# Kernel tuning notes

Measured on AMD Instinct MI355X. Metric: run time of the kernel, lower is better.

## Reference

```python
import jax, jax.numpy as jnp
import numpy as np

MARGIN = 0.4
GAMMA = 80.0
N = 4096
C = 64


def setup_inputs() -> dict:
    key = jax.random.key(0)
    k1, k2 = jax.random.split(key)
    similarity_matrix = jnp.tanh(jax.random.normal(k1, (N, N), dtype=jnp.float32))
    cluster_ids = jax.random.randint(k2, (N,), 0, C)
    clusters = jax.nn.one_hot(cluster_ids, C, dtype=jnp.float32)  # [N, C]
    return {"similarity_matrix": similarity_matrix, "clusters": clusters}


def reference(similarity_matrix, clusters):
    n = similarity_matrix.shape[0]
    # pairwise label dot products; original loop uses .item() -> detached weights
    prob = jax.lax.stop_gradient(clusters @ clusters.T)  # [n, n]
    upper = jnp.triu(jnp.ones((n, n), dtype=bool), k=1)
    pos = upper & (prob > 0)
    neg = upper & (prob <= 0)

    sim = similarity_matrix
    sim_d = jax.lax.stop_gradient(sim)
    ap = jnp.maximum(-sim_d + 1.0 + MARGIN, 0.0)
    an = jnp.maximum(sim_d + MARGIN, 0.0)
    delta_p = 1.0 - MARGIN
    delta_n = MARGIN
    logit_p = -ap * (sim - delta_p) * GAMMA
    logit_n = an * (sim - delta_n) * GAMMA

    neg_inf = jnp.float32(-jnp.inf)
    lse_p = jax.scipy.special.logsumexp(jnp.where(pos, logit_p, neg_inf))
    lse_n = jax.scipy.special.logsumexp(jnp.where(neg, logit_n, neg_inf))

    cnt_p = jnp.maximum(jnp.sum(pos), 1)
    cnt_n = jnp.maximum(jnp.sum(neg), 1)
    wp_mean = jnp.sum(jnp.where(pos, prob, 0.0)) / cnt_p
    wn_mean = jnp.sum(jnp.where(neg, prob, 0.0)) / cnt_n

    # mean over pairs of wp*softplus(lse_p) + wn*softplus(lse_n)
    loss = wp_mean * jax.nn.softplus(lse_p) + wn_mean * jax.nn.softplus(lse_n)
    return loss
```

## Files before the change

kernel.cpp:

```cpp
#include <hip/hip_runtime.h>
#include <math.h>

#define NN 4096
#define CC 64
#define CAP 256
#define QS 8
#define K3_THREADS 128

constexpr float K_MARGIN = 0.4f;
constexpr float K_GAMMA  = 80.0f;
constexpr float M_P = 307.2f;


__global__ void zero_kernel(int* __restrict__ cnt) {
    if (threadIdx.x < CC) cnt[threadIdx.x] = 0;
}

__global__ __launch_bounds__(256) void ids_bucket_kernel(const float* __restrict__ clusters,
                                                         int* __restrict__ cnt,
                                                         unsigned short* __restrict__ members) {
    const int row  = (blockIdx.x * 256 + threadIdx.x) >> 6;
    const int lane = threadIdx.x & 63;
    const float v = clusters[row * CC + lane];
    const unsigned long long m = __ballot(v > 0.5f);
    if (lane == 0) {
        const int id   = (int)__builtin_ctzll(m);
        const int slot = atomicAdd(&cnt[id], 1);
        members[id * CAP + slot] = (unsigned short)row;
    }
}

__global__ __launch_bounds__(K3_THREADS) void pairs_kernel(const float* __restrict__ sim,
                                                           const int* __restrict__ cnt,
                                                           const unsigned short* __restrict__ members,
                                                           float* __restrict__ partials) {
    const int c = blockIdx.x >> 3;
    const int q = blockIdx.x & (QS - 1);
    __shared__ int M[CAP];
    const int m = cnt[c];
    for (int t = threadIdx.x; t < m; t += K3_THREADS) M[t] = members[c * CAP + t];
    __syncthreads();

    float s_p = 0.f;
    for (int t = threadIdx.x; t < m; t += K3_THREADS) {
        const int r1 = M[t];
        for (int a = q; a < t; a += QS) {
            const int r0 = M[a];
            const int i2 = min(r0, r1);
            const int j2 = r0 ^ r1 ^ i2;
            const float s = sim[i2 * NN + j2];
            const float lp = -fmaxf(1.0f + K_MARGIN - s, 0.0f) * (s - (1.0f - K_MARGIN)) * K_GAMMA;
            s_p += __expf(lp - M_P);
        }
    }

    #pragma unroll
    for (int off = 32; off > 0; off >>= 1) s_p += __shfl_xor(s_p, off);
    __shared__ float red[2];
    const int wave = threadIdx.x >> 6;
    if ((threadIdx.x & 63) == 0) red[wave] = s_p;
    __syncthreads();
    if (threadIdx.x == 0) partials[blockIdx.x] = red[0] + red[1];
}

__device__ inline float softplus_f(float x) {
    return fmaxf(x, 0.0f) + log1pf(expf(-fabsf(x)));
}

__global__ __launch_bounds__(256) void final_kernel(const float* __restrict__ partials,
                                                    float* __restrict__ out) {
    float s = partials[threadIdx.x] + partials[threadIdx.x + 256];
    #pragma unroll
    for (int off = 32; off > 0; off >>= 1) s += __shfl_xor(s, off);
    __shared__ float red[4];
    const int wave = threadIdx.x >> 6;
    if ((threadIdx.x & 63) == 0) red[wave] = s;
    __syncthreads();
    if (threadIdx.x == 0) {
        const float S = red[0] + red[1] + red[2] + red[3];
        out[0] = softplus_f(logf(S) + M_P);
    }
}

extern "C" void kernel_launch(void* const* d_in, const int* in_sizes, int n_in,
                              void* d_out, int out_size, void* d_ws, size_t ws_size,
                              hipStream_t stream) {
    const float* sim      = (const float*)d_in[0];
    const float* clusters = (const float*)d_in[1];
    float* out = (float*)d_out;

    int*            cnt      = (int*)d_ws;
    unsigned short* members  = (unsigned short*)((char*)d_ws + 256);
    float*          partials = (float*)((char*)d_ws + 33024);

    zero_kernel<<<1, 64, 0, stream>>>(cnt);
    ids_bucket_kernel<<<(NN * 64) / 256, 256, 0, stream>>>(clusters, cnt, members);
    pairs_kernel<<<CC * QS, K3_THREADS, 0, stream>>>(sim, cnt, members, partials);
    final_kernel<<<1, 256, 0, stream>>>(partials, out);
}
```

Before: 115.3 us.

## Replace global-atomic bucketing with single-block shared-memory counting sort

Splits the cluster-id extraction from bucketing. A single 1024-thread block builds a compacted member list with shared-memory atomics and a prefix sum. This removes the separate zero kernel and the contended global atomics, and it also removes the fixed per-cluster capacity of 256. In exchange it adds a serial single-block launch and a 64-step scalar prefix loop.

```diff
diff --git a/kernel.cpp b/kernel.cpp
--- a/kernel.cpp
+++ b/kernel.cpp
@@ -3,7 +3,7 @@
 
 #define NN 4096
 #define CC 64
-#define CAP 256
+#define MAXM 512
 #define QS 8
 #define K3_THREADS 128
 
@@ -12,33 +12,60 @@
 constexpr float M_P = 307.2f;
 
 
-__global__ void zero_kernel(int* __restrict__ cnt) {
-    if (threadIdx.x < CC) cnt[threadIdx.x] = 0;
-}
-
-__global__ __launch_bounds__(256) void ids_bucket_kernel(const float* __restrict__ clusters,
-                                                         int* __restrict__ cnt,
-                                                         unsigned short* __restrict__ members) {
+__global__ __launch_bounds__(256) void ids_kernel(const float* __restrict__ clusters,
+                                                  int* __restrict__ ids) {
     const int row  = (blockIdx.x * 256 + threadIdx.x) >> 6;
     const int lane = threadIdx.x & 63;
     const float v = clusters[row * CC + lane];
     const unsigned long long m = __ballot(v > 0.5f);
-    if (lane == 0) {
-        const int id   = (int)__builtin_ctzll(m);
-        const int slot = atomicAdd(&cnt[id], 1);
-        members[id * CAP + slot] = (unsigned short)row;
+    if (lane == 0) ids[row] = (int)__builtin_ctzll(m);
+}
+
+__global__ __launch_bounds__(1024) void bucket_kernel(const int* __restrict__ ids,
+                                                      unsigned short* __restrict__ members,
+                                                      int* __restrict__ cntG,
+                                                      int* __restrict__ offG) {
+    __shared__ int cnt[CC];
+    __shared__ int off[CC];
+    __shared__ int place[CC];
+    const int t = threadIdx.x;
+    if (t < CC) cnt[t] = 0;
+    __syncthreads();
+
+    const int4 my = reinterpret_cast<const int4*>(ids)[t];
+    atomicAdd(&cnt[my.x], 1);
+    atomicAdd(&cnt[my.y], 1);
+    atomicAdd(&cnt[my.z], 1);
+    atomicAdd(&cnt[my.w], 1);
+    __syncthreads();
+
+    if (t == 0) {
+        int run = 0;
+        for (int c = 0; c < CC; ++c) { off[c] = run; place[c] = run; run += cnt[c]; }
     }
+    __syncthreads();
+
+    const int r0 = 4 * t;
+    int p;
+    p = atomicAdd(&place[my.x], 1); members[p] = (unsigned short)(r0 + 0);
+    p = atomicAdd(&place[my.y], 1); members[p] = (unsigned short)(r0 + 1);
+    p = atomicAdd(&place[my.z], 1); members[p] = (unsigned short)(r0 + 2);
+    p = atomicAdd(&place[my.w], 1); members[p] = (unsigned short)(r0 + 3);
+
+    if (t < CC) { cntG[t] = cnt[t]; offG[t] = off[t]; }
 }
 
 __global__ __launch_bounds__(K3_THREADS) void pairs_kernel(const float* __restrict__ sim,
-                                                           const int* __restrict__ cnt,
+                                                           const int* __restrict__ cntG,
+                                                           const int* __restrict__ offG,
                                                            const unsigned short* __restrict__ members,
                                                            float* __restrict__ partials) {
     const int c = blockIdx.x >> 3;
     const int q = blockIdx.x & (QS - 1);
-    __shared__ int M[CAP];
-    const int m = cnt[c];
-    for (int t = threadIdx.x; t < m; t += K3_THREADS) M[t] = members[c * CAP + t];
+    __shared__ int M[MAXM];
+    const int m    = cntG[c];
+    const int base = offG[c];
+    for (int t = threadIdx.x; t < m && t < MAXM; t += K3_THREADS) M[t] = members[base + t];
     __syncthreads();
 
     float s_p = 0.f;
@@ -57,8 +84,7 @@
     #pragma unroll
     for (int off = 32; off > 0; off >>= 1) s_p += __shfl_xor(s_p, off);
     __shared__ float red[2];
-    const int wave = threadIdx.x >> 6;
-    if ((threadIdx.x & 63) == 0) red[wave] = s_p;
+    if ((threadIdx.x & 63) == 0) red[threadIdx.x >> 6] = s_p;
     __syncthreads();
     if (threadIdx.x == 0) partials[blockIdx.x] = red[0] + red[1];
 }
@@ -73,8 +99,7 @@
     #pragma unroll
     for (int off = 32; off > 0; off >>= 1) s += __shfl_xor(s, off);
     __shared__ float red[4];
-    const int wave = threadIdx.x >> 6;
-    if ((threadIdx.x & 63) == 0) red[wave] = s;
+    if ((threadIdx.x & 63) == 0) red[threadIdx.x >> 6] = s;
     __syncthreads();
     if (threadIdx.x == 0) {
         const float S = red[0] + red[1] + red[2] + red[3];
@@ -89,12 +114,14 @@
     const float* clusters = (const float*)d_in[1];
     float* out = (float*)d_out;
 
-    int*            cnt      = (int*)d_ws;
-    unsigned short* members  = (unsigned short*)((char*)d_ws + 256);
-    float*          partials = (float*)((char*)d_ws + 33024);
+    int*            ids      = (int*)d_ws;
+    unsigned short* members  = (unsigned short*)((char*)d_ws + 16384);
+    int*            cntG     = (int*)((char*)d_ws + 24576);
+    int*            offG     = (int*)((char*)d_ws + 24832);
+    float*          partials = (float*)((char*)d_ws + 25088);
 
-    zero_kernel<<<1, 64, 0, stream>>>(cnt);
-    ids_bucket_kernel<<<(NN * 64) / 256, 256, 0, stream>>>(clusters, cnt, members);
-    pairs_kernel<<<CC * QS, K3_THREADS, 0, stream>>>(sim, cnt, members, partials);
+    ids_kernel<<<(NN * 64) / 256, 256, 0, stream>>>(clusters, ids);
+    bucket_kernel<<<1, 1024, 0, stream>>>(ids, members, cntG, offG);
+    pairs_kernel<<<CC * QS, K3_THREADS, 0, stream>>>(sim, cntG, offG, members, partials);
     final_kernel<<<1, 256, 0, stream>>>(partials, out);
 }
```

Measured after the change: 99.78 us. -13.5%, faster.
